# Kernel tuning notes

Measured on AMD Instinct MI355X. Metric: run time of the kernel, lower is better.

## Reference

```python
import jax, jax.numpy as jnp
import numpy as np

U, N, E, D = 200000, 50000, 1600000, 64


def setup_inputs() -> dict:
    key = jax.random.key(0)
    ks = jax.random.split(key, 8)
    nodes = jax.random.randint(ks[0], (N,), 0, U)
    neigh_idx = jax.random.randint(ks[1], (E,), 0, U)
    seg_ids = jnp.sort(jax.random.randint(ks[2], (E,), 0, N))
    u2e = jax.random.normal(ks[3], (U, D), dtype=jnp.float32) * 0.1
    W1 = jax.random.normal(ks[4], (2 * D, D), dtype=jnp.float32) * 0.1
    b1 = jnp.zeros((D,), dtype=jnp.float32)
    W2 = jax.random.normal(ks[5], (D, D), dtype=jnp.float32) * 0.1
    b2 = jnp.zeros((D,), dtype=jnp.float32)
    w3 = jax.random.normal(ks[6], (D, 1), dtype=jnp.float32) * 0.1
    b3 = jnp.zeros((1,), dtype=jnp.float32)
    return {"nodes": nodes, "neigh_idx": neigh_idx, "seg_ids": seg_ids,
            "u2e": u2e, "W1": W1, "b1": b1, "W2": W2, "b2": b2,
            "w3": w3, "b3": b3}


def reference(nodes, neigh_idx, seg_ids, u2e, W1, b1, W2, b2, w3, b3):
    # Per-node self representation  [N, D]
    u_rep = u2e[nodes]
    # Ragged neighbor gather flattened to edge list
    e_u = u2e[neigh_idx]                      # [E, D]
    u_edge = u_rep[seg_ids]                   # [E, D] node rep broadcast to its edges
    # Attention MLP (GraphRec-style), eval mode (no dropout)
    x = jnp.concatenate([e_u, u_edge], axis=1)            # [E, 2D]
    x = jax.nn.relu(x @ W1 + b1)
    x = jax.nn.relu(x @ W2 + b2)
    logits = (x @ w3 + b3)[:, 0]                           # [E]
    # Segment softmax over each node's neighbor set
    seg_max = jax.ops.segment_max(logits, seg_ids, num_segments=N)
    ex = jnp.exp(logits - seg_max[seg_ids])
    denom = jax.ops.segment_sum(ex, seg_ids, num_segments=N)
    att = ex / denom[seg_ids]                              # [E]
    # Attention-weighted neighbor aggregation: e_u^T @ att per node
    agg = jax.ops.segment_sum(att[:, None] * e_u, seg_ids, num_segments=N)  # [N, D]
    # Nodes with zero neighbors fall back to their own embedding
    counts = jax.ops.segment_sum(jnp.ones((E,), dtype=jnp.float32), seg_ids, num_segments=N)
    out = jnp.where(counts[:, None] > 0, agg, u_rep)
    return out
```

## Files before the change

### kernel.cpp

```cpp
#include <hip/hip_runtime.h>
#include <math.h>

#define D 64

typedef __fp16 fp16x2 __attribute__((ext_vector_type(2)));
typedef _Float16 half8 __attribute__((ext_vector_type(8)));
typedef _Float16 half4v __attribute__((ext_vector_type(4)));
typedef __attribute__((ext_vector_type(4))) float f32x4;

union h8pun { half8 v; fp16x2 h2[4]; };

__global__ __launch_bounds__(256) void k_proj_both(const float* __restrict__ u2e,
                                                   const int* __restrict__ nodes,
                                                   const float* __restrict__ W1,
                                                   const float* __restrict__ b1,
                                                   const float* __restrict__ W2,
                                                   _Float16* __restrict__ W2h,
                                                   const int* __restrict__ seg_ids,
                                                   int* __restrict__ start,
                                                   _Float16* __restrict__ q,
                                                   _Float16* __restrict__ u2e_h,
                                                   _Float16* __restrict__ p,
                                                   int U, int N, int E,
                                                   int wavesU, int wavesN) {
    int tid = blockIdx.x * blockDim.x + (int)threadIdx.x;
    if (tid <= N) {
        int lo = 0, hi = E;
        while (lo < hi) {
            int mid = (lo + hi) >> 1;
            if (seg_ids[mid] < tid) lo = mid + 1; else hi = mid;
        }
        start[tid] = lo;
    } else if (tid <= N + D * D) {
        int j = tid - (N + 1);
        int n = j >> 6, pos = j & 63;
        int k = (pos >> 2) + 16 * (pos & 3);
        W2h[n * D + pos] = (_Float16)W2[k * D + n];
    }

    int lane = threadIdx.x & 63;
    int m = lane & 15, quad = lane >> 4;
    int wave = (blockIdx.x * blockDim.x + threadIdx.x) >> 6;

    const int* idx;
    const float* bias;
    _Float16* outp;
    _Float16* copyp;
    int R, w0, wstride, w1off;
    if (wave < wavesU) {
        idx = nullptr; bias = nullptr; outp = q; copyp = u2e_h;
        R = U; w0 = wave; wstride = wavesU; w1off = 0;
    } else {
        idx = nodes; bias = b1; outp = p; copyp = nullptr;
        R = N; w0 = wave - wavesU; wstride = wavesN; w1off = D;
    }

    half8 Bf[2][4];
    float bv[4];
#pragma unroll
    for (int t = 0; t < 4; ++t) {
        int n = m + 16 * t;
        bv[t] = bias ? bias[n] : 0.0f;
#pragma unroll
        for (int kh = 0; kh < 2; ++kh) {
            int k0 = w1off + kh * 32 + quad * 8;
#pragma unroll
            for (int j = 0; j < 8; ++j) Bf[kh][t][j] = (_Float16)W1[(size_t)(k0 + j) * D + n];
        }
    }

    int ngroups = (R + 15) / 16;
    for (int g = w0; g < ngroups; g += wstride) {
        int r_ = g * 16 + m;
        int rs = r_ < R ? r_ : R - 1;
        int src = idx ? idx[rs] : rs;
        const float4* arow = (const float4*)(u2e + (size_t)src * D);
        float4 x0 = arow[quad * 2], x1 = arow[quad * 2 + 1];
        float4 y0 = arow[8 + quad * 2], y1 = arow[8 + quad * 2 + 1];
        h8pun A0, A1;
        A0.h2[0] = __builtin_amdgcn_cvt_pkrtz(x0.x, x0.y);
        A0.h2[1] = __builtin_amdgcn_cvt_pkrtz(x0.z, x0.w);
        A0.h2[2] = __builtin_amdgcn_cvt_pkrtz(x1.x, x1.y);
        A0.h2[3] = __builtin_amdgcn_cvt_pkrtz(x1.z, x1.w);
        A1.h2[0] = __builtin_amdgcn_cvt_pkrtz(y0.x, y0.y);
        A1.h2[1] = __builtin_amdgcn_cvt_pkrtz(y0.z, y0.w);
        A1.h2[2] = __builtin_amdgcn_cvt_pkrtz(y1.x, y1.y);
        A1.h2[3] = __builtin_amdgcn_cvt_pkrtz(y1.z, y1.w);
        if (copyp && r_ < R) {
            *(half8*)(copyp + (size_t)r_ * D + quad * 8) = A0.v;
            *(half8*)(copyp + (size_t)r_ * D + 32 + quad * 8) = A1.v;
        }
        f32x4 C[4];
#pragma unroll
        for (int t = 0; t < 4; ++t) C[t] = (f32x4){bv[t], bv[t], bv[t], bv[t]};
#pragma unroll
        for (int t = 0; t < 4; ++t) {
            C[t] = __builtin_amdgcn_mfma_f32_16x16x32_f16(A0.v, Bf[0][t], C[t], 0, 0, 0);
            C[t] = __builtin_amdgcn_mfma_f32_16x16x32_f16(A1.v, Bf[1][t], C[t], 0, 0, 0);
        }
#pragma unroll
        for (int r = 0; r < 4; ++r) {
            int row = g * 16 + quad * 4 + r;
            if (row < R) {
                half4v hv = {(_Float16)C[0][r], (_Float16)C[1][r],
                             (_Float16)C[2][r], (_Float16)C[3][r]};
                *(half4v*)(outp + (size_t)row * D + m * 4) = hv;
            }
        }
    }
}

__global__ __launch_bounds__(256) void k_edge_ex(const int* __restrict__ neigh_idx,
                                                 const int* __restrict__ seg_ids,
                                                 const _Float16* __restrict__ q,
                                                 const _Float16* __restrict__ p,
                                                 const _Float16* __restrict__ W2h,
                                                 const float* __restrict__ b2,
                                                 const float* __restrict__ w3,
                                                 const float* __restrict__ b3,
                                                 float* __restrict__ exb, int E) {
    int lane = threadIdx.x & 63;
    int m = lane & 15, quad = lane >> 4;

    half8 Bf[2][4];
    float b2v[4], w3v[4];
#pragma unroll
    for (int t = 0; t < 4; ++t) {
        int n = m + 16 * t;
        b2v[t] = b2[n];
        w3v[t] = w3[n];
        Bf[0][t] = *(const half8*)(W2h + n * D + quad * 8);
        Bf[1][t] = *(const half8*)(W2h + n * D + 32 + quad * 8);
    }
    float b3v = b3[0];
    const half8 hz = {0, 0, 0, 0, 0, 0, 0, 0};

    int ngroups = (E + 31) / 32;
    int wave = (blockIdx.x * blockDim.x + threadIdx.x) >> 6;
    int nwaves = (gridDim.x * blockDim.x) >> 6;

    int nbra = 0, sega = 0, nbrb = 0, segb = 0;
    if (wave < ngroups) {
        int ea = wave * 32 + m, eb = ea + 16;
        int eas = ea < E ? ea : E - 1;
        int ebs = eb < E ? eb : E - 1;
        nbra = neigh_idx[eas]; sega = seg_ids[eas];
        nbrb = neigh_idx[ebs]; segb = seg_ids[ebs];
    }
    for (int g = wave; g < ngroups; g += nwaves) {
        int gn = g + nwaves;
        int nbra_n = 0, sega_n = 0, nbrb_n = 0, segb_n = 0;
        if (gn < ngroups) {
            int ea = gn * 32 + m, eb = ea + 16;
            int eas = ea < E ? ea : E - 1;
            int ebs = eb < E ? eb : E - 1;
            nbra_n = neigh_idx[eas]; sega_n = seg_ids[eas];
            nbrb_n = neigh_idx[ebs]; segb_n = seg_ids[ebs];
        }
        const half8* qra = (const half8*)(q + (size_t)nbra * D);
        const half8* pra = (const half8*)(p + (size_t)sega * D);
        const half8* qrb = (const half8*)(q + (size_t)nbrb * D);
        const half8* prb = (const half8*)(p + (size_t)segb * D);
        half8 qa0 = qra[quad], qa1 = qra[quad + 4];
        half8 pa0 = pra[quad], pa1 = pra[quad + 4];
        half8 qb0 = qrb[quad], qb1 = qrb[quad + 4];
        half8 pb0 = prb[quad], pb1 = prb[quad + 4];
        half8 Aa0 = __builtin_elementwise_max(qa0 + pa0, hz);
        half8 Aa1 = __builtin_elementwise_max(qa1 + pa1, hz);
        half8 Ab0 = __builtin_elementwise_max(qb0 + pb0, hz);
        half8 Ab1 = __builtin_elementwise_max(qb1 + pb1, hz);
        f32x4 Ca[4], Cb[4];
#pragma unroll
        for (int t = 0; t < 4; ++t) {
            Ca[t] = (f32x4){b2v[t], b2v[t], b2v[t], b2v[t]};
            Cb[t] = Ca[t];
        }
#pragma unroll
        for (int t = 0; t < 4; ++t) {
            Ca[t] = __builtin_amdgcn_mfma_f32_16x16x32_f16(Aa0, Bf[0][t], Ca[t], 0, 0, 0);
            Ca[t] = __builtin_amdgcn_mfma_f32_16x16x32_f16(Aa1, Bf[1][t], Ca[t], 0, 0, 0);
            Cb[t] = __builtin_amdgcn_mfma_f32_16x16x32_f16(Ab0, Bf[0][t], Cb[t], 0, 0, 0);
            Cb[t] = __builtin_amdgcn_mfma_f32_16x16x32_f16(Ab1, Bf[1][t], Cb[t], 0, 0, 0);
        }
        float pa[4], pb[4];
#pragma unroll
        for (int r = 0; r < 4; ++r) {
            float sa = 0.0f, sb = 0.0f;
#pragma unroll
            for (int t = 0; t < 4; ++t) {
                sa += fmaxf(Ca[t][r], 0.0f) * w3v[t];
                sb += fmaxf(Cb[t][r], 0.0f) * w3v[t];
            }
            pa[r] = sa; pb[r] = sb;
        }
#pragma unroll
        for (int off = 1; off <= 8; off <<= 1) {
#pragma unroll
            for (int r = 0; r < 4; ++r) {
                pa[r] += __shfl_xor(pa[r], off, 64);
                pb[r] += __shfl_xor(pb[r], off, 64);
            }
        }
        if (m == 0) {
            int e0 = g * 32 + quad * 4;
            if (e0 + 3 < E)
                *(float4*)(exb + e0) = make_float4(__expf(pa[0] + b3v), __expf(pa[1] + b3v),
                                                   __expf(pa[2] + b3v), __expf(pa[3] + b3v));
            else
#pragma unroll
                for (int r = 0; r < 4; ++r)
                    if (e0 + r < E) exb[e0 + r] = __expf(pa[r] + b3v);
            int e1 = e0 + 16;
            if (e1 + 3 < E)
                *(float4*)(exb + e1) = make_float4(__expf(pb[0] + b3v), __expf(pb[1] + b3v),
                                                   __expf(pb[2] + b3v), __expf(pb[3] + b3v));
            else
#pragma unroll
                for (int r = 0; r < 4; ++r)
                    if (e1 + r < E) exb[e1 + r] = __expf(pb[r] + b3v);
        }
        nbra = nbra_n; sega = sega_n; nbrb = nbrb_n; segb = segb_n;
    }
}

__global__ __launch_bounds__(256) void k_agg_fast(const int* __restrict__ nodes,
                                                  const int* __restrict__ neigh_idx,
                                                  const float* __restrict__ u2e,
                                                  const _Float16* __restrict__ u2e_h,
                                                  const float* __restrict__ exb,
                                                  const int* __restrict__ start,
                                                  float* __restrict__ out, int N) {
    int n = blockIdx.x * 4 + ((int)threadIdx.x >> 6);
    int lane = threadIdx.x & 63;
    if (n >= N) return;
    int s = start[n];
    int t = start[n + 1];
    if (s == t) {
        int node = nodes[n];
        out[(size_t)n * D + lane] = u2e[(size_t)node * D + lane];
        return;
    }

    int grp = lane >> 3, sub = lane & 7;
    float acc[8];
#pragma unroll
    for (int j = 0; j < 8; ++j) acc[j] = 0.0f;
    float dsum = 0.0f;
    for (int i = s; i < t; i += 32) {
#pragma unroll
        for (int uu = 0; uu < 4; ++uu) {
            int ii = i + uu * 8 + grp;
            bool v = ii < t;
            int is = v ? ii : s;
            float w = exb[is];
            int nb = neigh_idx[is];
            half8 r = *(const half8*)(u2e_h + (size_t)nb * D + sub * 8);
            if (!v) w = 0.0f;
            dsum += w;
#pragma unroll
            for (int j = 0; j < 8; ++j) acc[j] += w * (float)r[j];
        }
    }
#pragma unroll
    for (int off = 8; off <= 32; off <<= 1) {
#pragma unroll
        for (int j = 0; j < 8; ++j) acc[j] += __shfl_xor(acc[j], off, 64);
        dsum += __shfl_xor(dsum, off, 64);
    }
    if (grp == 0) {
        float inv = 1.0f / dsum;
        float* o = out + (size_t)n * D + sub * 8;
        *(float4*)o = make_float4(acc[0] * inv, acc[1] * inv, acc[2] * inv, acc[3] * inv);
        *(float4*)(o + 4) = make_float4(acc[4] * inv, acc[5] * inv, acc[6] * inv, acc[7] * inv);
    }
}

extern "C" void kernel_launch(void* const* d_in, const int* in_sizes, int n_in,
                              void* d_out, int out_size, void* d_ws, size_t ws_size,
                              hipStream_t stream) {
    const int* nodes = (const int*)d_in[0];
    const int* neigh_idx = (const int*)d_in[1];
    const int* seg_ids = (const int*)d_in[2];
    const float* u2e = (const float*)d_in[3];
    const float* W1 = (const float*)d_in[4];
    const float* b1 = (const float*)d_in[5];
    const float* W2 = (const float*)d_in[6];
    const float* b2 = (const float*)d_in[7];
    const float* w3 = (const float*)d_in[8];
    const float* b3 = (const float*)d_in[9];
    float* out = (float*)d_out;

    int N = in_sizes[0];
    int E = in_sizes[1];
    int U = in_sizes[3] / D;

    char* ws = (char*)d_ws;
    size_t off = 0;
    auto alloc = [&](size_t bytes) {
        void* ptr = ws + off;
        off = (off + bytes + 255) & ~(size_t)255;
        return ptr;
    };
    float* exb = (float*)alloc((size_t)E * 4);
    int* start = (int*)alloc((size_t)(N + 1) * 4);
    _Float16* W2h = (_Float16*)alloc((size_t)D * D * 2);
    _Float16* q = (_Float16*)alloc((size_t)U * D * 2);
    _Float16* p = (_Float16*)alloc((size_t)N * D * 2);
    _Float16* u2e_h = (_Float16*)alloc((size_t)U * D * 2);
    (void)ws_size;

    const int wavesU = 6144, wavesN = 2048;
    k_proj_both<<<(wavesU + wavesN) / 4, 256, 0, stream>>>(u2e, nodes, W1, b1, W2, W2h,
                                                           seg_ids, start, q, u2e_h, p,
                                                           U, N, E, wavesU, wavesN);
    k_edge_ex<<<2048, 256, 0, stream>>>(neigh_idx, seg_ids, q, p, W2h,
                                        b2, w3, b3, exb, E);
    k_agg_fast<<<(N + 3) / 4, 256, 0, stream>>>(nodes, neigh_idx, u2e, u2e_h,
                                                exb, start, out, N);
}
```

Before: 209.6 us.

## Fuse edge logits and aggregation into one segment-chunked kernel

Merges the edge-logit kernel and the aggregation kernel into a single kernel. Each wave processes a chunk of whole segments, computes the first-layer projection of each neighbor on the fly with MFMA instead of precomputing q for all U rows, and accumulates the softmax-weighted sum directly without a max subtraction. This drops the q buffer, the exb buffer and one launch, and it avoids reading each neighbor row twice. In exchange it adds per-edge first-layer MFMA work, an LDS transpose round trip, a per-segment flush loop, and possible load imbalance from long segments that straddle chunks.

```diff
diff --git a/kernel.cpp b/kernel.cpp
--- a/kernel.cpp
+++ b/kernel.cpp
@@ -2,6 +2,8 @@
 #include <math.h>
 
 #define D 64
+#define CHUNK 128
+#define ROWP 68
 
 typedef __fp16 fp16x2 __attribute__((ext_vector_type(2)));
 typedef _Float16 half8 __attribute__((ext_vector_type(8)));
@@ -18,7 +20,6 @@
                                                    _Float16* __restrict__ W2h,
                                                    const int* __restrict__ seg_ids,
                                                    int* __restrict__ start,
-                                                   _Float16* __restrict__ q,
                                                    _Float16* __restrict__ u2e_h,
                                                    _Float16* __restrict__ p,
                                                    int U, int N, int E,
@@ -42,38 +43,48 @@
     int m = lane & 15, quad = lane >> 4;
     int wave = (blockIdx.x * blockDim.x + threadIdx.x) >> 6;
 
-    const int* idx;
-    const float* bias;
-    _Float16* outp;
-    _Float16* copyp;
-    int R, w0, wstride, w1off;
     if (wave < wavesU) {
-        idx = nullptr; bias = nullptr; outp = q; copyp = u2e_h;
-        R = U; w0 = wave; wstride = wavesU; w1off = 0;
-    } else {
-        idx = nodes; bias = b1; outp = p; copyp = nullptr;
-        R = N; w0 = wave - wavesU; wstride = wavesN; w1off = D;
-    }
-
+        int ngroups = (U + 15) / 16;
+        for (int g = wave; g < ngroups; g += wavesU) {
+            int r_ = g * 16 + m;
+            if (r_ >= U) continue;
+            const float4* arow = (const float4*)(u2e + (size_t)r_ * D);
+            float4 x0 = arow[quad * 2], x1 = arow[quad * 2 + 1];
+            float4 y0 = arow[8 + quad * 2], y1 = arow[8 + quad * 2 + 1];
+            h8pun A0, A1;
+            A0.h2[0] = __builtin_amdgcn_cvt_pkrtz(x0.x, x0.y);
+            A0.h2[1] = __builtin_amdgcn_cvt_pkrtz(x0.z, x0.w);
+            A0.h2[2] = __builtin_amdgcn_cvt_pkrtz(x1.x, x1.y);
+            A0.h2[3] = __builtin_amdgcn_cvt_pkrtz(x1.z, x1.w);
+            A1.h2[0] = __builtin_amdgcn_cvt_pkrtz(y0.x, y0.y);
+            A1.h2[1] = __builtin_amdgcn_cvt_pkrtz(y0.z, y0.w);
+            A1.h2[2] = __builtin_amdgcn_cvt_pkrtz(y1.x, y1.y);
+            A1.h2[3] = __builtin_amdgcn_cvt_pkrtz(y1.z, y1.w);
+            *(half8*)(u2e_h + (size_t)r_ * D + quad * 8) = A0.v;
+            *(half8*)(u2e_h + (size_t)r_ * D + 32 + quad * 8) = A1.v;
+        }
+        return;
+    }
+
+    int w0 = wave - wavesU;
     half8 Bf[2][4];
     float bv[4];
 #pragma unroll
     for (int t = 0; t < 4; ++t) {
         int n = m + 16 * t;
-        bv[t] = bias ? bias[n] : 0.0f;
+        bv[t] = b1[n];
 #pragma unroll
         for (int kh = 0; kh < 2; ++kh) {
-            int k0 = w1off + kh * 32 + quad * 8;
+            int k0 = D + kh * 32 + quad * 8;
 #pragma unroll
             for (int j = 0; j < 8; ++j) Bf[kh][t][j] = (_Float16)W1[(size_t)(k0 + j) * D + n];
         }
     }
-
-    int ngroups = (R + 15) / 16;
-    for (int g = w0; g < ngroups; g += wstride) {
+    int ngroups = (N + 15) / 16;
+    for (int g = w0; g < ngroups; g += wavesN) {
         int r_ = g * 16 + m;
-        int rs = r_ < R ? r_ : R - 1;
-        int src = idx ? idx[rs] : rs;
+        int rs = r_ < N ? r_ : N - 1;
+        int src = nodes[rs];
         const float4* arow = (const float4*)(u2e + (size_t)src * D);
         float4 x0 = arow[quad * 2], x1 = arow[quad * 2 + 1];
         float4 y0 = arow[8 + quad * 2], y1 = arow[8 + quad * 2 + 1];
@@ -86,10 +97,6 @@
         A1.h2[1] = __builtin_amdgcn_cvt_pkrtz(y0.z, y0.w);
         A1.h2[2] = __builtin_amdgcn_cvt_pkrtz(y1.x, y1.y);
         A1.h2[3] = __builtin_amdgcn_cvt_pkrtz(y1.z, y1.w);
-        if (copyp && r_ < R) {
-            *(half8*)(copyp + (size_t)r_ * D + quad * 8) = A0.v;
-            *(half8*)(copyp + (size_t)r_ * D + 32 + quad * 8) = A1.v;
-        }
         f32x4 C[4];
 #pragma unroll
         for (int t = 0; t < 4; ++t) C[t] = (f32x4){bv[t], bv[t], bv[t], bv[t]};
@@ -101,178 +108,192 @@
 #pragma unroll
         for (int r = 0; r < 4; ++r) {
             int row = g * 16 + quad * 4 + r;
-            if (row < R) {
+            if (row < N) {
                 half4v hv = {(_Float16)C[0][r], (_Float16)C[1][r],
                              (_Float16)C[2][r], (_Float16)C[3][r]};
-                *(half4v*)(outp + (size_t)row * D + m * 4) = hv;
+                *(half4v*)(p + (size_t)row * D + m * 4) = hv;
             }
         }
     }
 }
 
-__global__ __launch_bounds__(256) void k_edge_ex(const int* __restrict__ neigh_idx,
-                                                 const int* __restrict__ seg_ids,
-                                                 const _Float16* __restrict__ q,
-                                                 const _Float16* __restrict__ p,
-                                                 const _Float16* __restrict__ W2h,
-                                                 const float* __restrict__ b2,
-                                                 const float* __restrict__ w3,
-                                                 const float* __restrict__ b3,
-                                                 float* __restrict__ exb, int E) {
+__global__ __launch_bounds__(256) void k_edge_agg(const int* __restrict__ neigh_idx,
+                                                  const int* __restrict__ seg_ids,
+                                                  const _Float16* __restrict__ u2e_h,
+                                                  const _Float16* __restrict__ p,
+                                                  const _Float16* __restrict__ W2h,
+                                                  const float* __restrict__ W1,
+                                                  const float* __restrict__ b2,
+                                                  const float* __restrict__ w3,
+                                                  const float* __restrict__ b3,
+                                                  const int* __restrict__ start,
+                                                  const int* __restrict__ nodes,
+                                                  const float* __restrict__ u2e,
+                                                  float* __restrict__ out,
+                                                  int E, int N, int nchunks) {
+    __shared__ _Float16 lds_x[4][16 * ROWP];
+    int wib = (int)threadIdx.x >> 6;
+    _Float16* lx = lds_x[wib];
+
+    int tid = blockIdx.x * blockDim.x + (int)threadIdx.x;
+    if (tid < N) {
+        if (start[tid + 1] == start[tid]) {
+            const float4* src = (const float4*)(u2e + (size_t)nodes[tid] * D);
+            float4* dst = (float4*)(out + (size_t)tid * D);
+#pragma unroll
+            for (int j = 0; j < 16; ++j) dst[j] = src[j];
+        }
+    }
+
     int lane = threadIdx.x & 63;
     int m = lane & 15, quad = lane >> 4;
-
-    half8 Bf[2][4];
+    int wave = tid >> 6;
+    if (wave >= nchunks) return;
+    int e_lo = wave * CHUNK;
+
+    int lo = 0, hi = N + 1;
+    while (lo < hi) { int mid = (lo + hi) >> 1; if (start[mid] < e_lo) lo = mid + 1; else hi = mid; }
+    int s_begin = (lo <= N) ? start[lo] : E;
+    int bound = e_lo + CHUNK;
+    hi = N + 1;
+    while (lo < hi) { int mid = (lo + hi) >> 1; if (start[mid] < bound) lo = mid + 1; else hi = mid; }
+    int s_end = (lo <= N) ? start[lo] : E;
+    if (s_begin >= s_end) return;
+
+    half8 Bf1[2][4], Bf2[2][4];
     float b2v[4], w3v[4];
 #pragma unroll
     for (int t = 0; t < 4; ++t) {
         int n = m + 16 * t;
         b2v[t] = b2[n];
         w3v[t] = w3[n];
-        Bf[0][t] = *(const half8*)(W2h + n * D + quad * 8);
-        Bf[1][t] = *(const half8*)(W2h + n * D + 32 + quad * 8);
+        Bf2[0][t] = *(const half8*)(W2h + n * D + quad * 8);
+        Bf2[1][t] = *(const half8*)(W2h + n * D + 32 + quad * 8);
+#pragma unroll
+        for (int kh = 0; kh < 2; ++kh) {
+            int k0 = kh * 32 + quad * 8;
+#pragma unroll
+            for (int j = 0; j < 8; ++j) Bf1[kh][t][j] = (_Float16)W1[(size_t)(k0 + j) * D + n];
+        }
     }
     float b3v = b3[0];
     const half8 hz = {0, 0, 0, 0, 0, 0, 0, 0};
 
-    int ngroups = (E + 31) / 32;
-    int wave = (blockIdx.x * blockDim.x + threadIdx.x) >> 6;
-    int nwaves = (gridDim.x * blockDim.x) >> 6;
-
-    int nbra = 0, sega = 0, nbrb = 0, segb = 0;
-    if (wave < ngroups) {
-        int ea = wave * 32 + m, eb = ea + 16;
-        int eas = ea < E ? ea : E - 1;
-        int ebs = eb < E ? eb : E - 1;
-        nbra = neigh_idx[eas]; sega = seg_ids[eas];
-        nbrb = neigh_idx[ebs]; segb = seg_ids[ebs];
-    }
-    for (int g = wave; g < ngroups; g += nwaves) {
-        int gn = g + nwaves;
-        int nbra_n = 0, sega_n = 0, nbrb_n = 0, segb_n = 0;
-        if (gn < ngroups) {
-            int ea = gn * 32 + m, eb = ea + 16;
-            int eas = ea < E ? ea : E - 1;
-            int ebs = eb < E ? eb : E - 1;
-            nbra_n = neigh_idx[eas]; sega_n = seg_ids[eas];
-            nbrb_n = neigh_idx[ebs]; segb_n = seg_ids[ebs];
-        }
-        const half8* qra = (const half8*)(q + (size_t)nbra * D);
-        const half8* pra = (const half8*)(p + (size_t)sega * D);
-        const half8* qrb = (const half8*)(q + (size_t)nbrb * D);
-        const half8* prb = (const half8*)(p + (size_t)segb * D);
-        half8 qa0 = qra[quad], qa1 = qra[quad + 4];
-        half8 pa0 = pra[quad], pa1 = pra[quad + 4];
-        half8 qb0 = qrb[quad], qb1 = qrb[quad + 4];
-        half8 pb0 = prb[quad], pb1 = prb[quad + 4];
-        half8 Aa0 = __builtin_elementwise_max(qa0 + pa0, hz);
-        half8 Aa1 = __builtin_elementwise_max(qa1 + pa1, hz);
-        half8 Ab0 = __builtin_elementwise_max(qb0 + pb0, hz);
-        half8 Ab1 = __builtin_elementwise_max(qb1 + pb1, hz);
-        f32x4 Ca[4], Cb[4];
+    int cur_seg = seg_ids[s_begin];
+    float acc0[8], acc1[8], dsum = 0.0f;
+    bool dirty = false;
+#pragma unroll
+    for (int j = 0; j < 8; ++j) { acc0[j] = 0.0f; acc1[j] = 0.0f; }
+
+    auto flush = [&]() {
+#pragma unroll
+        for (int off = 1; off <= 8; off <<= 1) {
+#pragma unroll
+            for (int j = 0; j < 8; ++j) {
+                acc0[j] += __shfl_xor(acc0[j], off, 64);
+                acc1[j] += __shfl_xor(acc1[j], off, 64);
+            }
+            dsum += __shfl_xor(dsum, off, 64);
+        }
+        if (m == 0) {
+            float inv = 1.0f / dsum;
+            float* o = out + (size_t)cur_seg * D + quad * 8;
+            *(float4*)o = make_float4(acc0[0] * inv, acc0[1] * inv, acc0[2] * inv, acc0[3] * inv);
+            *(float4*)(o + 4) = make_float4(acc0[4] * inv, acc0[5] * inv, acc0[6] * inv, acc0[7] * inv);
+            float* o2 = o + 32;
+            *(float4*)o2 = make_float4(acc1[0] * inv, acc1[1] * inv, acc1[2] * inv, acc1[3] * inv);
+            *(float4*)(o2 + 4) = make_float4(acc1[4] * inv, acc1[5] * inv, acc1[6] * inv, acc1[7] * inv);
+        }
+#pragma unroll
+        for (int j = 0; j < 8; ++j) { acc0[j] = 0.0f; acc1[j] = 0.0f; }
+        dsum = 0.0f;
+        dirty = false;
+    };
+
+    int ec0 = s_begin + m; if (ec0 > s_end - 1) ec0 = s_end - 1;
+    int nb = neigh_idx[ec0], sg = seg_ids[ec0];
+
+    for (int e0 = s_begin; e0 < s_end; e0 += 16) {
+        int nb_c = nb, sg_c = sg;
+        bool valid = (e0 + m) < s_end;
+        int e1 = e0 + 16;
+        if (e1 < s_end) {
+            int ec = e1 + m; if (ec > s_end - 1) ec = s_end - 1;
+            nb = neigh_idx[ec]; sg = seg_ids[ec];
+        }
+        const half8* ur = (const half8*)(u2e_h + (size_t)nb_c * D);
+        half8 ua0 = ur[quad], ua1 = ur[quad + 4];
+        const half8* pr = (const half8*)(p + (size_t)sg_c * D);
+        half8 pa0 = pr[quad], pa1 = pr[quad + 4];
+        f32x4 Cq[4];
+#pragma unroll
+        for (int t = 0; t < 4; ++t) Cq[t] = (f32x4){0.0f, 0.0f, 0.0f, 0.0f};
 #pragma unroll
         for (int t = 0; t < 4; ++t) {
-            Ca[t] = (f32x4){b2v[t], b2v[t], b2v[t], b2v[t]};
-            Cb[t] = Ca[t];
-        }
+            Cq[t] = __builtin_amdgcn_mfma_f32_16x16x32_f16(ua0, Bf1[0][t], Cq[t], 0, 0, 0);
+            Cq[t] = __builtin_amdgcn_mfma_f32_16x16x32_f16(ua1, Bf1[1][t], Cq[t], 0, 0, 0);
+        }
+#pragma unroll
+        for (int r = 0; r < 4; ++r) {
+            half4v hv = {(_Float16)Cq[0][r], (_Float16)Cq[1][r],
+                         (_Float16)Cq[2][r], (_Float16)Cq[3][r]};
+            *(half4v*)(lx + (quad * 4 + r) * ROWP + m * 4) = hv;
+        }
+        asm volatile("s_waitcnt lgkmcnt(0)" ::: "memory");
+        half8 xq0 = *(const half8*)(lx + m * ROWP + quad * 8);
+        half8 xq1 = *(const half8*)(lx + m * ROWP + 32 + quad * 8);
+        half8 x0 = __builtin_elementwise_max(xq0 + pa0, hz);
+        half8 x1 = __builtin_elementwise_max(xq1 + pa1, hz);
+        f32x4 Cl[4];
+#pragma unroll
+        for (int t = 0; t < 4; ++t) Cl[t] = (f32x4){b2v[t], b2v[t], b2v[t], b2v[t]};
 #pragma unroll
         for (int t = 0; t < 4; ++t) {
-            Ca[t] = __builtin_amdgcn_mfma_f32_16x16x32_f16(Aa0, Bf[0][t], Ca[t], 0, 0, 0);
-            Ca[t] = __builtin_amdgcn_mfma_f32_16x16x32_f16(Aa1, Bf[1][t], Ca[t], 0, 0, 0);
-            Cb[t] = __builtin_amdgcn_mfma_f32_16x16x32_f16(Ab0, Bf[0][t], Cb[t], 0, 0, 0);
-            Cb[t] = __builtin_amdgcn_mfma_f32_16x16x32_f16(Ab1, Bf[1][t], Cb[t], 0, 0, 0);
-        }
-        float pa[4], pb[4];
+            Cl[t] = __builtin_amdgcn_mfma_f32_16x16x32_f16(x0, Bf2[0][t], Cl[t], 0, 0, 0);
+            Cl[t] = __builtin_amdgcn_mfma_f32_16x16x32_f16(x1, Bf2[1][t], Cl[t], 0, 0, 0);
+        }
+        float pl[4];
 #pragma unroll
         for (int r = 0; r < 4; ++r) {
-            float sa = 0.0f, sb = 0.0f;
-#pragma unroll
-            for (int t = 0; t < 4; ++t) {
-                sa += fmaxf(Ca[t][r], 0.0f) * w3v[t];
-                sb += fmaxf(Cb[t][r], 0.0f) * w3v[t];
+            float s = 0.0f;
+#pragma unroll
+            for (int t = 0; t < 4; ++t) s += fmaxf(Cl[t][r], 0.0f) * w3v[t];
+            pl[r] = s;
+        }
+#pragma unroll
+        for (int off = 1; off <= 8; off <<= 1) {
+#pragma unroll
+            for (int r = 0; r < 4; ++r) pl[r] += __shfl_xor(pl[r], off, 64);
+        }
+        int srcl = (m >> 2) << 4;
+        float t0 = __shfl(pl[0], srcl, 64), t1 = __shfl(pl[1], srcl, 64);
+        float t2 = __shfl(pl[2], srcl, 64), t3 = __shfl(pl[3], srcl, 64);
+        int rr = m & 3;
+        float lg = rr == 0 ? t0 : rr == 1 ? t1 : rr == 2 ? t2 : t3;
+        float exm = __expf(lg + b3v);
+        int sgw = valid ? sg_c : 0x7fffffff;
+        bool active = valid;
+        while (__any(active)) {
+            int s0 = active ? sgw : 0x7fffffff;
+#pragma unroll
+            for (int off = 1; off <= 8; off <<= 1) s0 = min(s0, __shfl_xor(s0, off, 64));
+            if (s0 != cur_seg) {
+                if (dirty) flush();
+                cur_seg = s0;
             }
-            pa[r] = sa; pb[r] = sb;
-        }
-#pragma unroll
-        for (int off = 1; off <= 8; off <<= 1) {
-#pragma unroll
-            for (int r = 0; r < 4; ++r) {
-                pa[r] += __shfl_xor(pa[r], off, 64);
-                pb[r] += __shfl_xor(pb[r], off, 64);
+            bool mine = active && (sgw == s0);
+            float w = mine ? exm : 0.0f;
+            dsum += w;
+#pragma unroll
+            for (int j = 0; j < 8; ++j) {
+                acc0[j] += w * (float)ua0[j];
+                acc1[j] += w * (float)ua1[j];
             }
-        }
-        if (m == 0) {
-            int e0 = g * 32 + quad * 4;
-            if (e0 + 3 < E)
-                *(float4*)(exb + e0) = make_float4(__expf(pa[0] + b3v), __expf(pa[1] + b3v),
-                                                   __expf(pa[2] + b3v), __expf(pa[3] + b3v));
-            else
-#pragma unroll
-                for (int r = 0; r < 4; ++r)
-                    if (e0 + r < E) exb[e0 + r] = __expf(pa[r] + b3v);
-            int e1 = e0 + 16;
-            if (e1 + 3 < E)
-                *(float4*)(exb + e1) = make_float4(__expf(pb[0] + b3v), __expf(pb[1] + b3v),
-                                                   __expf(pb[2] + b3v), __expf(pb[3] + b3v));
-            else
-#pragma unroll
-                for (int r = 0; r < 4; ++r)
-                    if (e1 + r < E) exb[e1 + r] = __expf(pb[r] + b3v);
-        }
-        nbra = nbra_n; sega = sega_n; nbrb = nbrb_n; segb = segb_n;
-    }
-}
-
-__global__ __launch_bounds__(256) void k_agg_fast(const int* __restrict__ nodes,
-                                                  const int* __restrict__ neigh_idx,
-                                                  const float* __restrict__ u2e,
-                                                  const _Float16* __restrict__ u2e_h,
-                                                  const float* __restrict__ exb,
-                                                  const int* __restrict__ start,
-                                                  float* __restrict__ out, int N) {
-    int n = blockIdx.x * 4 + ((int)threadIdx.x >> 6);
-    int lane = threadIdx.x & 63;
-    if (n >= N) return;
-    int s = start[n];
-    int t = start[n + 1];
-    if (s == t) {
-        int node = nodes[n];
-        out[(size_t)n * D + lane] = u2e[(size_t)node * D + lane];
-        return;
-    }
-
-    int grp = lane >> 3, sub = lane & 7;
-    float acc[8];
-#pragma unroll
-    for (int j = 0; j < 8; ++j) acc[j] = 0.0f;
-    float dsum = 0.0f;
-    for (int i = s; i < t; i += 32) {
-#pragma unroll
-        for (int uu = 0; uu < 4; ++uu) {
-            int ii = i + uu * 8 + grp;
-            bool v = ii < t;
-            int is = v ? ii : s;
-            float w = exb[is];
-            int nb = neigh_idx[is];
-            half8 r = *(const half8*)(u2e_h + (size_t)nb * D + sub * 8);
-            if (!v) w = 0.0f;
-            dsum += w;
-#pragma unroll
-            for (int j = 0; j < 8; ++j) acc[j] += w * (float)r[j];
-        }
-    }
-#pragma unroll
-    for (int off = 8; off <= 32; off <<= 1) {
-#pragma unroll
-        for (int j = 0; j < 8; ++j) acc[j] += __shfl_xor(acc[j], off, 64);
-        dsum += __shfl_xor(dsum, off, 64);
-    }
-    if (grp == 0) {
-        float inv = 1.0f / dsum;
-        float* o = out + (size_t)n * D + sub * 8;
-        *(float4*)o = make_float4(acc[0] * inv, acc[1] * inv, acc[2] * inv, acc[3] * inv);
-        *(float4*)(o + 4) = make_float4(acc[4] * inv, acc[5] * inv, acc[6] * inv, acc[7] * inv);
-    }
+            dirty = true;
+            active = active && !mine;
+        }
+    }
+    if (dirty) flush();
 }
 
 extern "C" void kernel_launch(void* const* d_in, const int* in_sizes, int n_in,
@@ -294,6 +315,8 @@
     int E = in_sizes[1];
     int U = in_sizes[3] / D;
 
+    int nchunks = (E + CHUNK - 1) / CHUNK;
+
     char* ws = (char*)d_ws;
     size_t off = 0;
     auto alloc = [&](size_t bytes) {
@@ -301,20 +324,17 @@
         off = (off + bytes + 255) & ~(size_t)255;
         return ptr;
     };
-    float* exb = (float*)alloc((size_t)E * 4);
     int* start = (int*)alloc((size_t)(N + 1) * 4);
     _Float16* W2h = (_Float16*)alloc((size_t)D * D * 2);
-    _Float16* q = (_Float16*)alloc((size_t)U * D * 2);
     _Float16* p = (_Float16*)alloc((size_t)N * D * 2);
     _Float16* u2e_h = (_Float16*)alloc((size_t)U * D * 2);
     (void)ws_size;
 
     const int wavesU = 6144, wavesN = 2048;
     k_proj_both<<<(wavesU + wavesN) / 4, 256, 0, stream>>>(u2e, nodes, W1, b1, W2, W2h,
-                                                           seg_ids, start, q, u2e_h, p,
+                                                           seg_ids, start, u2e_h, p,
                                                            U, N, E, wavesU, wavesN);
-    k_edge_ex<<<2048, 256, 0, stream>>>(neigh_idx, seg_ids, q, p, W2h,
-                                        b2, w3, b3, exb, E);
-    k_agg_fast<<<(N + 3) / 4, 256, 0, stream>>>(nodes, neigh_idx, u2e, u2e_h,
-                                                exb, start, out, N);
+    k_edge_agg<<<(nchunks + 3) / 4, 256, 0, stream>>>(neigh_idx, seg_ids, u2e_h, p,
+                                                      W2h, W1, b2, w3, b3, start,
+                                                      nodes, u2e, out, E, N, nchunks);
 }
```

Result: slower. 325.8 us (+55.5%).
